# Kernel optimization log

Hardware: AMD Instinct MI355X
Metric: run time of the kernel (lower is better)

## Reference

```python
import math
import jax, jax.numpy as jnp
import numpy as np

B, H, S, D = 4, 16, 2048, 64

def setup_inputs() -> dict:
    key = jax.random.key(0)
    kq, kk, kv, km = jax.random.split(key, 4)
    q = jax.random.normal(kq, (B, H, S, D), dtype=jnp.float32)
    k = jax.random.normal(kk, (B, H, S, D), dtype=jnp.float32)
    v = jax.random.normal(kv, (B, H, S, D), dtype=jnp.float32)
    mask = jax.random.randint(km, (B, 1, S, S), 0, 2, dtype=jnp.int32)
    return {"q": q, "k": k, "v": v, "mask": mask}

def reference(q, k, v, mask):
    d_k = q.shape[-1]
    # score: [B, H, S, S] = Q @ K^T / sqrt(d_k)
    score = jnp.einsum('bhqd,bhkd->bhqk', q, k) / math.sqrt(d_k)
    # faithful to original: masked positions filled with 1e-12 (not -inf) before softmax
    score = jnp.where(mask == 0, jnp.float32(1e-12), score)
    score = jax.nn.softmax(score, axis=-1)
    output = jnp.einsum('bhqk,bhkd->bhqd', score, v)
    return output, score
```

## Files before the change

### kernel.cpp

```cpp
#include <hip/hip_runtime.h>
#include <stdint.h>

#define BATCH 4
#define HEADS 16
#define SEQ   2048
#define DIM   64
#define QT    32
#define KT    64
#define EST   72

typedef __attribute__((ext_vector_type(8))) short  short8;
typedef __attribute__((ext_vector_type(4))) short  short4v;
typedef __attribute__((ext_vector_type(4))) float  floatx4;
typedef __attribute__((ext_vector_type(4))) int    intx4;

static __device__ __forceinline__ unsigned short f32_to_bf16_bits(float f) {
    union { float f; uint32_t u; } x; x.f = f;
    uint32_t r = x.u + 0x7FFFu + ((x.u >> 16) & 1u);
    return (unsigned short)(r >> 16);
}

__global__ __launch_bounds__(256, 4) void attn_fused_kernel(
    const float* __restrict__ q, const float* __restrict__ k,
    const float* __restrict__ v, const int* __restrict__ mask,
    float* __restrict__ out, float* __restrict__ score)
{
    __shared__ __align__(16) unsigned short Es[2][QT][EST];
    __shared__ float lsum[QT];

    const int tid  = threadIdx.x;
    const int w    = tid >> 6;
    const int lane = tid & 63;
    const int quad = lane >> 4;
    const int nl   = lane & 15;

    const int qt = blockIdx.x;
    const int bh = blockIdx.y;
    const int b  = bh >> 4;
    const int q0 = qt * QT;

    const float* kbase = k + (size_t)bh * SEQ * DIM;
    const float* vbase = v + (size_t)bh * SEQ * DIM;
    const int*   mbase = mask + ((size_t)b * SEQ + q0) * SEQ;

    if (tid < QT) lsum[tid] = 0.0f;

    short8 aq[2][2];
    {
        const float* qp = q + ((size_t)bh * SEQ + q0) * DIM;
        #pragma unroll
        for (int mt = 0; mt < 2; ++mt) {
            const float* qrow = qp + (size_t)(mt * 16 + nl) * DIM + quad * 8;
            #pragma unroll
            for (int s = 0; s < 2; ++s) {
                floatx4 f0 = *(const floatx4*)(qrow + s * 32);
                floatx4 f1 = *(const floatx4*)(qrow + s * 32 + 4);
                short8 a;
                #pragma unroll
                for (int j = 0; j < 4; ++j) {
                    a[j]     = (short)f32_to_bf16_bits(f0[j]);
                    a[j + 4] = (short)f32_to_bf16_bits(f1[j]);
                }
                aq[mt][s] = a;
            }
        }
    }

    float   rs[2]   = {0.f, 0.f};
    floatx4 oacc[2] = {{0.f,0.f,0.f,0.f},{0.f,0.f,0.f,0.f}};

    for (int t = 0; t < SEQ / KT; ++t) {
        const int k0 = t * KT;
        const int p  = t & 1;

        float vraw[2][8];
        {
            const float* vp = vbase + ((size_t)k0 + quad * 8) * DIM + w * 16 + nl;
            #pragma unroll
            for (int s = 0; s < 2; ++s)
                #pragma unroll
                for (int j = 0; j < 8; ++j)
                    vraw[s][j] = vp[(s * 32 + j) * DIM];
        }

        short8 kf[2];
        {
            const float* krow = kbase + (size_t)(k0 + w * 16 + nl) * DIM + quad * 8;
            #pragma unroll
            for (int s = 0; s < 2; ++s) {
                floatx4 f0 = *(const floatx4*)(krow + s * 32);
                floatx4 f1 = *(const floatx4*)(krow + s * 32 + 4);
                short8 kk;
                #pragma unroll
                for (int j = 0; j < 4; ++j) {
                    kk[j]     = (short)f32_to_bf16_bits(f0[j]);
                    kk[j + 4] = (short)f32_to_bf16_bits(f1[j]);
                }
                kf[s] = kk;
            }
        }

        intx4 mr[2];
        #pragma unroll
        for (int mt = 0; mt < 2; ++mt)
            mr[mt] = *(const intx4*)(mbase + (size_t)(mt * 16 + nl) * SEQ + k0 + w * 16 + quad * 4);

        floatx4 acc[2] = {{0.f,0.f,0.f,0.f},{0.f,0.f,0.f,0.f}};
        #pragma unroll
        for (int mt = 0; mt < 2; ++mt)
            #pragma unroll
            for (int s = 0; s < 2; ++s)
                acc[mt] = __builtin_amdgcn_mfma_f32_16x16x32_bf16(kf[s], aq[mt][s], acc[mt], 0, 0, 0);

        #pragma unroll
        for (int mt = 0; mt < 2; ++mt) {
            short4v es;
            float esum = 0.f;
            #pragma unroll
            for (int i = 0; i < 4; ++i) {
                float e = (mr[mt][i] != 0) ? __expf(acc[mt][i] * 0.125f) : 1.0f;
                esum += e;
                es[i] = (short)f32_to_bf16_bits(e);
            }
            rs[mt] += esum;
            *(short4v*)&Es[p][mt * 16 + nl][w * 16 + quad * 4] = es;
        }

        __syncthreads();

        #pragma unroll
        for (int s = 0; s < 2; ++s) {
            short8 vf;
            #pragma unroll
            for (int j = 0; j < 8; ++j)
                vf[j] = (short)f32_to_bf16_bits(vraw[s][j]);
            #pragma unroll
            for (int mt = 0; mt < 2; ++mt) {
                short8 ef = *(const short8*)&Es[p][mt * 16 + nl][s * 32 + quad * 8];
                oacc[mt] = __builtin_amdgcn_mfma_f32_16x16x32_bf16(vf, ef, oacc[mt], 0, 0, 0);
            }
        }
    }

    #pragma unroll
    for (int mt = 0; mt < 2; ++mt) {
        float x = rs[mt];
        x += __shfl_xor(x, 16);
        x += __shfl_xor(x, 32);
        if (quad == 0) atomicAdd(&lsum[mt * 16 + nl], x);
    }
    __syncthreads();
    if (tid < QT) lsum[tid] = 1.0f / lsum[tid];
    __syncthreads();
    const float rcp[2] = { lsum[nl], lsum[16 + nl] };

    #pragma unroll
    for (int mt = 0; mt < 2; ++mt) {
        floatx4 o;
        #pragma unroll
        for (int i = 0; i < 4; ++i) o[i] = oacc[mt][i] * rcp[mt];
        *(floatx4*)&out[((size_t)bh * SEQ + q0 + mt * 16 + nl) * DIM + w * 16 + quad * 4] = o;
    }

    float* sb = score + ((size_t)bh * SEQ + q0) * SEQ;
    for (int t = 0; t < SEQ / KT; ++t) {
        const int k0 = t * KT;

        short8 kf[2];
        {
            const float* krow = kbase + (size_t)(k0 + w * 16 + nl) * DIM + quad * 8;
            #pragma unroll
            for (int s = 0; s < 2; ++s) {
                floatx4 f0 = *(const floatx4*)(krow + s * 32);
                floatx4 f1 = *(const floatx4*)(krow + s * 32 + 4);
                short8 kk;
                #pragma unroll
                for (int j = 0; j < 4; ++j) {
                    kk[j]     = (short)f32_to_bf16_bits(f0[j]);
                    kk[j + 4] = (short)f32_to_bf16_bits(f1[j]);
                }
                kf[s] = kk;
            }
        }
        intx4 mr[2];
        #pragma unroll
        for (int mt = 0; mt < 2; ++mt)
            mr[mt] = *(const intx4*)(mbase + (size_t)(mt * 16 + nl) * SEQ + k0 + w * 16 + quad * 4);

        floatx4 acc[2] = {{0.f,0.f,0.f,0.f},{0.f,0.f,0.f,0.f}};
        #pragma unroll
        for (int mt = 0; mt < 2; ++mt)
            #pragma unroll
            for (int s = 0; s < 2; ++s)
                acc[mt] = __builtin_amdgcn_mfma_f32_16x16x32_bf16(kf[s], aq[mt][s], acc[mt], 0, 0, 0);

        #pragma unroll
        for (int mt = 0; mt < 2; ++mt) {
            floatx4 sv;
            #pragma unroll
            for (int i = 0; i < 4; ++i) {
                float e = (mr[mt][i] != 0) ? __expf(acc[mt][i] * 0.125f) : 1.0f;
                sv[i] = e * rcp[mt];
            }
            *(floatx4*)&sb[(size_t)(mt * 16 + nl) * SEQ + k0 + w * 16 + quad * 4] = sv;
        }
    }
}

extern "C" void kernel_launch(void* const* d_in, const int* in_sizes, int n_in,
                              void* d_out, int out_size, void* d_ws, size_t ws_size,
                              hipStream_t stream) {
    (void)in_sizes; (void)n_in; (void)out_size; (void)d_ws; (void)ws_size;
    const float* q    = (const float*)d_in[0];
    const float* k    = (const float*)d_in[1];
    const float* v    = (const float*)d_in[2];
    const int*   mask = (const int*)d_in[3];
    float* out   = (float*)d_out;
    float* score = out + (size_t)BATCH * HEADS * SEQ * DIM;
    dim3 grid(SEQ / QT, BATCH * HEADS);
    attn_fused_kernel<<<grid, dim3(256), 0, stream>>>(q, k, v, mask, out, score);
}
```

Before: 1.807 ms.

## Pre-convert K/V to bf16 with transposed V and double the query tile

Adds a prepass kernel that converts K to bf16 and writes V transposed in bf16 into workspace, so the main kernel loads MFMA operands as contiguous short8 vectors. This replaces per-tile fp32 loads, conversions and strided V gathers. The query tile also grows from 32 to 64 rows, which halves how often K/V are re-read across the grid. The cost is an extra launch, workspace traffic, more registers per thread and fewer blocks in the grid.

```diff
diff --git a/kernel.cpp b/kernel.cpp
--- a/kernel.cpp
+++ b/kernel.cpp
@@ -5,7 +5,8 @@
 #define HEADS 16
 #define SEQ   2048
 #define DIM   64
-#define QT    32
+#define QT    64
+#define MT    4
 #define KT    64
 #define EST   72
 
@@ -20,9 +21,59 @@
     return (unsigned short)(r >> 16);
 }
 
+__global__ __launch_bounds__(256) void prepass_kernel(
+    const float* __restrict__ k, const float* __restrict__ v,
+    unsigned short* __restrict__ kbf, unsigned short* __restrict__ vt)
+{
+    __shared__ unsigned short T[64][72];
+    const int tid = threadIdx.x;
+    const int r   = tid >> 2;
+    const int cb  = (tid & 3) * 16;
+    const int k0  = blockIdx.x * 64;
+    const int bh  = blockIdx.y;
+
+    const size_t rowoff = ((size_t)bh * SEQ + k0 + r) * DIM + cb;
+
+    {
+        const floatx4* kp = (const floatx4*)(k + rowoff);
+        floatx4 f0 = kp[0], f1 = kp[1], f2 = kp[2], f3 = kp[3];
+        short8 o0, o1;
+        #pragma unroll
+        for (int j = 0; j < 4; ++j) {
+            o0[j]     = (short)f32_to_bf16_bits(f0[j]);
+            o0[j + 4] = (short)f32_to_bf16_bits(f1[j]);
+            o1[j]     = (short)f32_to_bf16_bits(f2[j]);
+            o1[j + 4] = (short)f32_to_bf16_bits(f3[j]);
+        }
+        *(short8*)&kbf[rowoff]     = o0;
+        *(short8*)&kbf[rowoff + 8] = o1;
+    }
+    {
+        const floatx4* vp = (const floatx4*)(v + rowoff);
+        floatx4 f0 = vp[0], f1 = vp[1], f2 = vp[2], f3 = vp[3];
+        #pragma unroll
+        for (int j = 0; j < 4; ++j) {
+            T[cb + j][r]      = f32_to_bf16_bits(f0[j]);
+            T[cb + 4 + j][r]  = f32_to_bf16_bits(f1[j]);
+            T[cb + 8 + j][r]  = f32_to_bf16_bits(f2[j]);
+            T[cb + 12 + j][r] = f32_to_bf16_bits(f3[j]);
+        }
+    }
+    __syncthreads();
+    {
+        short8 t0 = *(const short8*)&T[r][cb];
+        short8 t1 = *(const short8*)&T[r][cb + 8];
+        unsigned short* dst = vt + ((size_t)bh * DIM + r) * SEQ + k0 + cb;
+        *(short8*)dst       = t0;
+        *(short8*)(dst + 8) = t1;
+    }
+}
+
+template <bool PRE>
 __global__ __launch_bounds__(256, 4) void attn_fused_kernel(
     const float* __restrict__ q, const float* __restrict__ k,
     const float* __restrict__ v, const int* __restrict__ mask,
+    const unsigned short* __restrict__ kbf, const unsigned short* __restrict__ vt,
     float* __restrict__ out, float* __restrict__ score)
 {
     __shared__ __align__(16) unsigned short Es[2][QT][EST];
@@ -41,15 +92,17 @@
 
     const float* kbase = k + (size_t)bh * SEQ * DIM;
     const float* vbase = v + (size_t)bh * SEQ * DIM;
-    const int*   mbase = mask + ((size_t)b * SEQ + q0) * SEQ;
+    const unsigned short* kbbase = PRE ? kbf + ((size_t)bh * SEQ + w * 16 + nl) * DIM + quad * 8 : nullptr;
+    const unsigned short* vtbase = PRE ? vt + ((size_t)bh * DIM + w * 16 + nl) * SEQ + quad * 8 : nullptr;
+    const int* mbase = mask + ((size_t)b * SEQ + q0) * SEQ;
 
     if (tid < QT) lsum[tid] = 0.0f;
 
-    short8 aq[2][2];
+    short8 aq[MT][2];
     {
         const float* qp = q + ((size_t)bh * SEQ + q0) * DIM;
         #pragma unroll
-        for (int mt = 0; mt < 2; ++mt) {
+        for (int mt = 0; mt < MT; ++mt) {
             const float* qrow = qp + (size_t)(mt * 16 + nl) * DIM + quad * 8;
             #pragma unroll
             for (int s = 0; s < 2; ++s) {
@@ -66,25 +119,19 @@
         }
     }
 
-    float   rs[2]   = {0.f, 0.f};
-    floatx4 oacc[2] = {{0.f,0.f,0.f,0.f},{0.f,0.f,0.f,0.f}};
+    float   rs[MT]   = {0.f, 0.f, 0.f, 0.f};
+    floatx4 oacc[MT] = {{0.f,0.f,0.f,0.f},{0.f,0.f,0.f,0.f},{0.f,0.f,0.f,0.f},{0.f,0.f,0.f,0.f}};
 
     for (int t = 0; t < SEQ / KT; ++t) {
         const int k0 = t * KT;
         const int p  = t & 1;
 
-        float vraw[2][8];
-        {
-            const float* vp = vbase + ((size_t)k0 + quad * 8) * DIM + w * 16 + nl;
-            #pragma unroll
-            for (int s = 0; s < 2; ++s)
-                #pragma unroll
-                for (int j = 0; j < 8; ++j)
-                    vraw[s][j] = vp[(s * 32 + j) * DIM];
-        }
-
         short8 kf[2];
-        {
+        if constexpr (PRE) {
+            const unsigned short* kp = kbbase + (size_t)k0 * DIM;
+            kf[0] = *(const short8*)kp;
+            kf[1] = *(const short8*)(kp + 32);
+        } else {
             const float* krow = kbase + (size_t)(k0 + w * 16 + nl) * DIM + quad * 8;
             #pragma unroll
             for (int s = 0; s < 2; ++s) {
@@ -99,21 +146,37 @@
                 kf[s] = kk;
             }
         }
-
-        intx4 mr[2];
-        #pragma unroll
-        for (int mt = 0; mt < 2; ++mt)
+        short8 vf[2];
+        if constexpr (PRE) {
+            const unsigned short* vp = vtbase + k0;
+            vf[0] = *(const short8*)vp;
+            vf[1] = *(const short8*)(vp + 32);
+        } else {
+            const float* vp = vbase + ((size_t)k0 + quad * 8) * DIM + w * 16 + nl;
+            #pragma unroll
+            for (int s = 0; s < 2; ++s) {
+                short8 vv;
+                #pragma unroll
+                for (int j = 0; j < 8; ++j)
+                    vv[j] = (short)f32_to_bf16_bits(vp[(s * 32 + j) * DIM]);
+                vf[s] = vv;
+            }
+        }
+
+        intx4 mr[MT];
+        #pragma unroll
+        for (int mt = 0; mt < MT; ++mt)
             mr[mt] = *(const intx4*)(mbase + (size_t)(mt * 16 + nl) * SEQ + k0 + w * 16 + quad * 4);
 
-        floatx4 acc[2] = {{0.f,0.f,0.f,0.f},{0.f,0.f,0.f,0.f}};
-        #pragma unroll
-        for (int mt = 0; mt < 2; ++mt)
+        floatx4 acc[MT] = {{0.f,0.f,0.f,0.f},{0.f,0.f,0.f,0.f},{0.f,0.f,0.f,0.f},{0.f,0.f,0.f,0.f}};
+        #pragma unroll
+        for (int mt = 0; mt < MT; ++mt)
             #pragma unroll
             for (int s = 0; s < 2; ++s)
                 acc[mt] = __builtin_amdgcn_mfma_f32_16x16x32_bf16(kf[s], aq[mt][s], acc[mt], 0, 0, 0);
 
         #pragma unroll
-        for (int mt = 0; mt < 2; ++mt) {
+        for (int mt = 0; mt < MT; ++mt) {
             short4v es;
             float esum = 0.f;
             #pragma unroll
@@ -129,21 +192,16 @@
         __syncthreads();
 
         #pragma unroll
-        for (int s = 0; s < 2; ++s) {
-            short8 vf;
-            #pragma unroll
-            for (int j = 0; j < 8; ++j)
-                vf[j] = (short)f32_to_bf16_bits(vraw[s][j]);
-            #pragma unroll
-            for (int mt = 0; mt < 2; ++mt) {
+        for (int s = 0; s < 2; ++s)
+            #pragma unroll
+            for (int mt = 0; mt < MT; ++mt) {
                 short8 ef = *(const short8*)&Es[p][mt * 16 + nl][s * 32 + quad * 8];
-                oacc[mt] = __builtin_amdgcn_mfma_f32_16x16x32_bf16(vf, ef, oacc[mt], 0, 0, 0);
-            }
-        }
+                oacc[mt] = __builtin_amdgcn_mfma_f32_16x16x32_bf16(vf[s], ef, oacc[mt], 0, 0, 0);
+            }
     }
 
     #pragma unroll
-    for (int mt = 0; mt < 2; ++mt) {
+    for (int mt = 0; mt < MT; ++mt) {
         float x = rs[mt];
         x += __shfl_xor(x, 16);
         x += __shfl_xor(x, 32);
@@ -152,10 +210,10 @@
     __syncthreads();
     if (tid < QT) lsum[tid] = 1.0f / lsum[tid];
     __syncthreads();
-    const float rcp[2] = { lsum[nl], lsum[16 + nl] };
+    const float rcp[MT] = { lsum[nl], lsum[16 + nl], lsum[32 + nl], lsum[48 + nl] };
 
     #pragma unroll
-    for (int mt = 0; mt < 2; ++mt) {
+    for (int mt = 0; mt < MT; ++mt) {
         floatx4 o;
         #pragma unroll
         for (int i = 0; i < 4; ++i) o[i] = oacc[mt][i] * rcp[mt];
@@ -167,7 +225,11 @@
         const int k0 = t * KT;
 
         short8 kf[2];
-        {
+        if constexpr (PRE) {
+            const unsigned short* kp = kbbase + (size_t)k0 * DIM;
+            kf[0] = *(const short8*)kp;
+            kf[1] = *(const short8*)(kp + 32);
+        } else {
             const float* krow = kbase + (size_t)(k0 + w * 16 + nl) * DIM + quad * 8;
             #pragma unroll
             for (int s = 0; s < 2; ++s) {
@@ -182,20 +244,20 @@
                 kf[s] = kk;
             }
         }
-        intx4 mr[2];
-        #pragma unroll
-        for (int mt = 0; mt < 2; ++mt)
+        intx4 mr[MT];
+        #pragma unroll
+        for (int mt = 0; mt < MT; ++mt)
             mr[mt] = *(const intx4*)(mbase + (size_t)(mt * 16 + nl) * SEQ + k0 + w * 16 + quad * 4);
 
-        floatx4 acc[2] = {{0.f,0.f,0.f,0.f},{0.f,0.f,0.f,0.f}};
-        #pragma unroll
-        for (int mt = 0; mt < 2; ++mt)
+        floatx4 acc[MT] = {{0.f,0.f,0.f,0.f},{0.f,0.f,0.f,0.f},{0.f,0.f,0.f,0.f},{0.f,0.f,0.f,0.f}};
+        #pragma unroll
+        for (int mt = 0; mt < MT; ++mt)
             #pragma unroll
             for (int s = 0; s < 2; ++s)
                 acc[mt] = __builtin_amdgcn_mfma_f32_16x16x32_bf16(kf[s], aq[mt][s], acc[mt], 0, 0, 0);
 
         #pragma unroll
-        for (int mt = 0; mt < 2; ++mt) {
+        for (int mt = 0; mt < MT; ++mt) {
             floatx4 sv;
             #pragma unroll
             for (int i = 0; i < 4; ++i) {
@@ -210,13 +272,24 @@
 extern "C" void kernel_launch(void* const* d_in, const int* in_sizes, int n_in,
                               void* d_out, int out_size, void* d_ws, size_t ws_size,
                               hipStream_t stream) {
-    (void)in_sizes; (void)n_in; (void)out_size; (void)d_ws; (void)ws_size;
+    (void)in_sizes; (void)n_in; (void)out_size;
     const float* q    = (const float*)d_in[0];
     const float* k    = (const float*)d_in[1];
     const float* v    = (const float*)d_in[2];
     const int*   mask = (const int*)d_in[3];
     float* out   = (float*)d_out;
     float* score = out + (size_t)BATCH * HEADS * SEQ * DIM;
+
+    const size_t elems = (size_t)BATCH * HEADS * SEQ * DIM;
+    const size_t need  = elems * 2 * 2;
     dim3 grid(SEQ / QT, BATCH * HEADS);
-    attn_fused_kernel<<<grid, dim3(256), 0, stream>>>(q, k, v, mask, out, score);
-}
+
+    if (d_ws != nullptr && ws_size >= need) {
+        unsigned short* kbf = (unsigned short*)d_ws;
+        unsigned short* vtp = kbf + elems;
+        prepass_kernel<<<dim3(SEQ / 64, BATCH * HEADS), dim3(256), 0, stream>>>(k, v, kbf, vtp);
+        attn_fused_kernel<true><<<grid, dim3(256), 0, stream>>>(q, k, v, mask, kbf, vtp, out, score);
+    } else {
+        attn_fused_kernel<false><<<grid, dim3(256), 0, stream>>>(q, k, v, mask, nullptr, nullptr, out, score);
+    }
+}
```

Measured after the change: 1.685 ms. -6.7%, faster.
